# Optimization experiments

Measured on AMD Instinct MI355X. Metric: run time of the kernel, lower is better.

## Reference

```python
import jax, jax.numpy as jnp
import numpy as np

NUM_GAUSS = 64
MAX_R = 5.0
ANG_TO_NM = 0.1  # du.ANG_TO_NM_SCALE
L = 4
C_NODE = 256
C_HID = 256
MAX_ATOMS = 100
B = 512      # building blocks
NPB = 32     # atoms per block
K = 20       # max_neighbors
N = B * NPB
E = N * K
GAUSS_COEFF = -0.5 / (MAX_R / (NUM_GAUSS - 1)) ** 2


def setup_inputs() -> dict:
    rng = np.random.default_rng(0)
    # all atoms of a block inside a 2.5A cube -> every pair within MAX_R=5A,
    # so radius_graph capped at K neighbors == K-nearest graph (fixed E).
    pos = (rng.random((B, NPB, 3)) * 2.5).astype(np.float32)
    d = np.linalg.norm(pos[:, :, None, :] - pos[:, None, :, :], axis=-1)  # [B,n,n]
    ii = np.arange(NPB)
    d[:, ii, ii] = np.inf  # loop=False
    nbr = np.argsort(d, axis=-1)[:, :, :K]  # [B,n,K] nearest neighbors
    base = (np.arange(B) * NPB)[:, None, None]
    row = np.broadcast_to(ii[None, :, None], (B, NPB, K)) + base
    col = nbr + base
    edge_index = np.stack([row.reshape(-1), col.reshape(-1)]).astype(np.int64)

    key = jax.random.key(0)
    ks = jax.random.split(key, 8)

    def lin(k, fi, fo):
        return jax.random.normal(k, (L, fi, fo), jnp.float32) / np.sqrt(fi).astype(np.float32)

    d_e_in = 2 * C_NODE + 1 + NUM_GAUSS  # 577
    return {
        'local_coords': jnp.asarray(pos.reshape(N, 3)),
        'atom_types': jax.random.randint(ks[0], (N,), 1, MAX_ATOMS + 1),  # 1..max_atoms
        'edge_index': jnp.asarray(edge_index),
        'batch_bb': jnp.repeat(jnp.arange(B, dtype=jnp.int32), NPB),
        'atom_embed': jax.random.normal(ks[1], (MAX_ATOMS, C_NODE), jnp.float32) * 0.1,
        'offset': jnp.linspace(0.0, MAX_R, NUM_GAUSS, dtype=jnp.float32),
        'We1': lin(ks[2], d_e_in, C_HID), 'be1': jnp.zeros((L, C_HID), jnp.float32),
        'We2': lin(ks[3], C_HID, C_HID), 'be2': jnp.zeros((L, C_HID), jnp.float32),
        'Wn1': lin(ks[4], C_HID + C_NODE, C_HID), 'bn1': jnp.zeros((L, C_HID), jnp.float32),
        'Wn2': lin(ks[5], C_HID, C_NODE), 'bn2': jnp.zeros((L, C_NODE), jnp.float32),
    }


def _forward(local_coords, atom_types, edge_index, batch_bb, atom_embed, offset,
             We1, be1, We2, be2, Wn1, bn1, Wn2, bn2):
    row, col = edge_index[0], edge_index[1]
    h = atom_embed[atom_types - 1]                      # [N, C_NODE]
    # Gaussian smearing of pairwise distances (Angstrom)
    dvec = local_coords[col] - local_coords[row]        # [E, 3]
    dist = jnp.sqrt(jnp.sum(dvec * dvec, axis=-1))      # [E]
    edge_attr = jnp.exp(GAUSS_COEFF * (dist[:, None] - offset[None, :]) ** 2)  # [E, 64]
    coord = local_coords * ANG_TO_NM
    cdiff = coord[row] - coord[col]
    radial = jnp.sum(cdiff * cdiff, axis=-1, keepdims=True)  # [E, 1]
    nblocks = batch_bb.shape[0] // NPB  # static
    for l in range(L):  # small fixed layer count
        e_in = jnp.concatenate([h[row], h[col], radial, edge_attr], axis=-1)  # [E, 577]
        m = jax.nn.relu(e_in @ We1[l] + be1[l])
        m = jax.nn.relu(m @ We2[l] + be2[l])                 # edge_mlp output [E, C_HID]
        agg = jax.ops.segment_sum(m, row, num_segments=N)    # scatter-sum to nodes
        n_in = jnp.concatenate([h, agg], axis=-1)            # [N, C_NODE + C_HID]
        out = jax.nn.relu(n_in @ Wn1[l] + bn1[l]) @ Wn2[l] + bn2[l]
        node_update = h + out                                # residual inside E_GCL
        h = h + node_update                                  # outer residual in forward
    # global_mean_pool over building blocks
    s = jax.ops.segment_sum(h, batch_bb, num_segments=B)
    cnt = jax.ops.segment_sum(jnp.ones((h.shape[0], 1), h.dtype), batch_bb, num_segments=B)
    return s / cnt


def reference(local_coords, atom_types, edge_index, batch_bb, atom_embed, offset,
              We1, be1, We2, be2, Wn1, bn1, Wn2, bn2):
    return _forward(local_coords, atom_types, edge_index, batch_bb, atom_embed, offset,
                    We1, be1, We2, be2, Wn1, bn1, Wn2, bn2)
```

## Files before the change

### kernel.cpp

```cpp
#include <hip/hip_runtime.h>
#include <hip/hip_bf16.h>
#include <stdint.h>

#define NATOMS 16384
#define ETOT   327680
#define NLAYER 4

typedef __hip_bfloat16 bf16;
using bf16x8 = __attribute__((ext_vector_type(8))) short;
using bf16x4 = __attribute__((ext_vector_type(4))) short;
using f32x4  = __attribute__((ext_vector_type(4))) float;

#define LDSF_STRIDE 260

__device__ __forceinline__ float bf2f(short s) {
  union { float f; unsigned u; } x; x.u = ((unsigned)(unsigned short)s) << 16; return x.f;
}
__device__ __forceinline__ short f2bf(float f) {
  bf16 b = __float2bfloat16(f);
  return *(short*)&b;
}

__device__ __forceinline__ void async16(const void* g, void* l) {
  __builtin_amdgcn_global_load_lds(
      (const __attribute__((address_space(1))) unsigned int*)g,
      (__attribute__((address_space(3))) unsigned int*)l, 16, 0, 0);
}

template<int KTOT, int EPI, int MT>
__global__ void __launch_bounds__(256, 2)
gemm_k(const bf16* A, const bf16* A2, const bf16* B,
       bf16* Obf, int ldOut, const float* bias,
       float* Hf, bf16* Hbf)
{
  __shared__ __align__(16) char smem[49152];
  __shared__ float s_bias[256];

  const int tid  = threadIdx.x;
  const int w    = tid >> 6;
  const int lane = tid & 63;
  const int q    = lane >> 4;
  const int t16  = lane & 15;
  const size_t row0 = (size_t)blockIdx.x * MT;
  const int ncol0 = blockIdx.y * 256;
  constexpr int MI = MT / 16;
  constexpr int AI = MT / 32;

  if constexpr (EPI == 2 || EPI == 4) s_bias[tid] = bias[tid];

  f32x4 acc[MI][4] = {};

  constexpr int NCHUNK = KTOT / 64;
  for (int kc = 0; kc < NCHUNK; ++kc) {
    const int k0 = kc * 64;
    const bf16* Asrc; int k0e; int ldA;
    if constexpr (KTOT == 512) {
      if (k0 < 256) { Asrc = A;  k0e = k0;       }
      else          { Asrc = A2; k0e = k0 - 256; }
      ldA = 256;
    } else {
      Asrc = A; k0e = k0; ldA = KTOT;
    }

    __syncthreads();
    #pragma unroll
    for (int ii = 0; ii < AI; ++ii) {
      int i = w * AI + ii;
      int f = i * 64 + lane;
      int m = f >> 3, s = f & 7;
      int ko = s ^ (m & 7);
      const bf16* g = Asrc + (row0 + (size_t)m) * ldA + (size_t)(k0e + ko * 8);
      async16(g, smem + i * 1024);
    }
    #pragma unroll
    for (int ii = 0; ii < 8; ++ii) {
      int i = w * 8 + ii;
      int f = i * 64 + lane;
      int n = f >> 3, s = f & 7;
      int ko = s ^ (n & 7);
      const bf16* g = B + (size_t)(ncol0 + n) * KTOT + (size_t)(k0 + ko * 8);
      async16(g, smem + 16384 + i * 1024);
    }
    __syncthreads();

    #pragma unroll
    for (int ks = 0; ks < 2; ++ks) {
      bf16x8 av[MI]; bf16x8 bv[4];
      const int ko = q + 4 * ks;
      #pragma unroll
      for (int mi = 0; mi < MI; ++mi) {
        int m = 16 * mi + t16;
        int f = m * 8 + (ko ^ (m & 7));
        av[mi] = *(const bf16x8*)(smem + f * 16);
      }
      #pragma unroll
      for (int ni = 0; ni < 4; ++ni) {
        int n = 64 * w + 16 * ni + t16;
        int f = n * 8 + (ko ^ (n & 7));
        bv[ni] = *(const bf16x8*)(smem + 16384 + f * 16);
      }
      #pragma unroll
      for (int mi = 0; mi < MI; ++mi)
        #pragma unroll
        for (int ni = 0; ni < 4; ++ni)
          acc[mi][ni] = __builtin_amdgcn_mfma_f32_16x16x32_bf16(
              av[mi], bv[ni], acc[mi][ni], 0, 0, 0);
    }
  }

  float* lds_f = (float*)smem;
  #pragma unroll
  for (int mi = 0; mi < MI; ++mi) {
    __syncthreads();
    #pragma unroll
    for (int ni = 0; ni < 4; ++ni)
      #pragma unroll
      for (int r = 0; r < 4; ++r)
        lds_f[(4 * q + r) * LDSF_STRIDE + 64 * w + 16 * ni + t16] = acc[mi][ni][r];
    __syncthreads();
    #pragma unroll
    for (int j = 0; j < 2; ++j) {
      int task = tid + 256 * j;
      int rr = task >> 5, cg = task & 31;
      int c0 = cg * 8;
      size_t rg = row0 + 16 * mi + rr;
      f32x4 v0 = *(const f32x4*)(lds_f + rr * LDSF_STRIDE + c0);
      f32x4 v1 = *(const f32x4*)(lds_f + rr * LDSF_STRIDE + c0 + 4);
      float v[8] = {v0[0], v0[1], v0[2], v0[3], v1[0], v1[1], v1[2], v1[3]};
      if constexpr (EPI == 0) {
        bf16x8 o;
        #pragma unroll
        for (int k = 0; k < 8; ++k) o[k] = f2bf(v[k]);
        *(bf16x8*)(Obf + rg * ldOut + (ncol0 + c0)) = o;
      } else if constexpr (EPI == 2) {
        bf16x8 o;
        #pragma unroll
        for (int k = 0; k < 8; ++k) o[k] = f2bf(fmaxf(v[k] + s_bias[c0 + k], 0.f));
        *(bf16x8*)(Obf + rg * 256 + c0) = o;
      } else {
        f32x4 h0 = *(const f32x4*)(Hf + rg * 256 + c0);
        f32x4 h1 = *(const f32x4*)(Hf + rg * 256 + c0 + 4);
        float hh[8] = {h0[0], h0[1], h0[2], h0[3], h1[0], h1[1], h1[2], h1[3]};
        bf16x8 o; f32x4 n0, n1;
        #pragma unroll
        for (int k = 0; k < 8; ++k) {
          float hn = 2.f * hh[k] + v[k] + s_bias[c0 + k];
          o[k] = f2bf(hn);
          if (k < 4) n0[k] = hn; else n1[k - 4] = hn;
        }
        *(f32x4*)(Hf + rg * 256 + c0)     = n0;
        *(f32x4*)(Hf + rg * 256 + c0 + 4) = n1;
        *(bf16x8*)(Hbf + rg * 256 + c0) = o;
      }
    }
  }
}

#define WINC 40960
#define WINR 57856
#define SCOL 59968
#define SRAD 60288
#define WPITCH 528

__global__ void __launch_bounds__(256, 2)
edge_fused(const bf16* Wgp_l, const bf16* W2p_l, const float* off,
           const float* pos, const int* eidx, const bf16* Prc,
           const float* be1, const float* wrad, const float* be2, bf16* Agg)
{
  __shared__ __align__(16) char smem[60608];
  int*   s_col = (int*)  (smem + SCOL);
  float* s_rad = (float*)(smem + SRAD);

  const int tid  = threadIdx.x;
  const int w    = tid >> 6;
  const int lane = tid & 63;
  const int q    = lane >> 4;
  const int t16  = lane & 15;
  const int blk  = blockIdx.x;
  const int node0  = (blk >> 3) * 32;
  const int rnode0 = blk * 4;
  const int ebase  = blk * 80;

  bf16x8 wgf[4][2];
  #pragma unroll
  for (int fi = 0; fi < 4; ++fi)
    #pragma unroll
    for (int ks = 0; ks < 2; ++ks)
      wgf[fi][ks] = *(const bf16x8*)(Wgp_l + (size_t)(((fi * 2 + ks) * 4 + w) * 512)
                                     + lane * 8);

  {
    int row = tid >> 3, seg = tid & 7;
    const bf16* src = Prc + (size_t)(node0 + row) * 512 + 256 + seg * 32;
    char* dst = smem + WINC + row * WPITCH + seg * 64;
    #pragma unroll
    for (int j = 0; j < 4; ++j)
      *(bf16x8*)(dst + j * 16) = *(const bf16x8*)(src + j * 8);
  }
  if (tid < 128) {
    int row = tid >> 5, seg = tid & 31;
    *(bf16x8*)(smem + WINR + row * WPITCH + seg * 16) =
        *(const bf16x8*)(Prc + (size_t)(rnode0 + row) * 512 + seg * 8);
  }

  if (tid < 80) {
    int e = ebase + tid;
    int rg = rnode0 + tid / 20;
    int cg = eidx[ETOT + e];
    float dx = pos[cg * 3 + 0] - pos[rg * 3 + 0];
    float dy = pos[cg * 3 + 1] - pos[rg * 3 + 1];
    float dz = pos[cg * 3 + 2] - pos[rg * 3 + 2];
    float d2 = dx * dx + dy * dy + dz * dz;
    s_col[tid] = cg & 31;
    s_rad[tid] = 0.01f * d2;
    float d = sqrtf(d2);
    const float GC = -0.5f / ((5.0f / 63.0f) * (5.0f / 63.0f));
    #pragma unroll
    for (int oct = 0; oct < 8; ++oct) {
      bf16x8 v;
      #pragma unroll
      for (int j = 0; j < 8; ++j) {
        float t = d - off[oct * 8 + j];
        v[j] = f2bf(__expf(GC * t * t));
      }
      int f = tid * 8 + (oct ^ (tid & 7));
      *(bf16x8*)(smem + f * 16) = v;
    }
  }
  __syncthreads();

  f32x4 acc1[4][5] = {};
  #pragma unroll
  for (int ks = 0; ks < 2; ++ks) {
    const int ko = q + 4 * ks;
    bf16x8 gv[5];
    #pragma unroll
    for (int ci = 0; ci < 5; ++ci) {
      int e = 16 * ci + t16;
      int f = e * 8 + (ko ^ (e & 7));
      gv[ci] = *(const bf16x8*)(smem + f * 16);
    }
    #pragma unroll
    for (int fi = 0; fi < 4; ++fi)
      #pragma unroll
      for (int ci = 0; ci < 5; ++ci)
        acc1[fi][ci] = __builtin_amdgcn_mfma_f32_16x16x32_bf16(
            wgf[fi][ks], gv[ci], acc1[fi][ci], 0, 0, 0);
  }
  __syncthreads();

  {
    f32x4 tb[4], tw[4];
    #pragma unroll
    for (int fi = 0; fi < 4; ++fi) {
      int fb = 64 * w + 16 * fi + 4 * q;
      tb[fi] = *(const f32x4*)(be1 + fb);
      tw[fi] = *(const f32x4*)(wrad + fb);
    }
    #pragma unroll
    for (int ci = 0; ci < 5; ++ci) {
      int e = 16 * ci + t16;
      int rl = e / 20;
      int cl = s_col[e];
      float rad = s_rad[e];
      #pragma unroll
      for (int fi = 0; fi < 4; ++fi) {
        int fb = 64 * w + 16 * fi + 4 * q;
        bf16x4 pr = *(const bf16x4*)(smem + WINR + rl * WPITCH + fb * 2);
        bf16x4 pc = *(const bf16x4*)(smem + WINC + cl * WPITCH + fb * 2);
        bf16x4 o;
        #pragma unroll
        for (int r = 0; r < 4; ++r) {
          float val = acc1[fi][ci][r] + tb[fi][r] + rad * tw[fi][r]
                    + bf2f(pr[r]) + bf2f(pc[r]);
          o[r] = f2bf(fmaxf(val, 0.f));
        }
        int u = (16 * w + 4 * fi + q) ^ (e & 14);
        *(bf16x4*)(smem + e * 512 + u * 8) = o;
      }
    }
  }
  __syncthreads();

  f32x4 acc2[5][4] = {};
  #pragma unroll
  for (int kc = 0; kc < 4; ++kc) {
    bf16x8 bv[4][2];
    #pragma unroll
    for (int ni = 0; ni < 4; ++ni)
      #pragma unroll
      for (int ks = 0; ks < 2; ++ks) {
        int frag = kc * 8 + ks * 4 + ni;
        bv[ni][ks] = *(const bf16x8*)(W2p_l + (size_t)((frag * 4 + w) * 512)
                                      + lane * 8);
      }
    #pragma unroll
    for (int ks = 0; ks < 2; ++ks) {
      const int ko = q + 4 * ks;
      bf16x8 av[5];
      #pragma unroll
      for (int mi = 0; mi < 5; ++mi) {
        int e = 16 * mi + t16;
        int ub = (2 * (8 * kc + ko)) ^ (t16 & 14);
        av[mi] = *(const bf16x8*)(smem + e * 512 + ub * 8);
      }
      #pragma unroll
      for (int mi = 0; mi < 5; ++mi)
        #pragma unroll
        for (int ni = 0; ni < 4; ++ni)
          acc2[mi][ni] = __builtin_amdgcn_mfma_f32_16x16x32_bf16(
              av[mi], bv[ni][ks], acc2[mi][ni], 0, 0, 0);
    }
  }

  #pragma unroll
  for (int ni = 0; ni < 4; ++ni) {
    float b = be2[64 * w + 16 * ni + t16];
    float pp[5];
    #pragma unroll
    for (int mi = 0; mi < 5; ++mi) {
      float s = 0.f;
      #pragma unroll
      for (int r = 0; r < 4; ++r) s += fmaxf(acc2[mi][ni][r] + b, 0.f);
      pp[mi] = s;
    }
    #pragma unroll
    for (int nn = 0; nn < 4; ++nn) {
      float s = 0.f;
      #pragma unroll
      for (int mi = 0; mi < 5; ++mi) {
        int g = 4 * mi + q;
        if (g >= 5 * nn && g <= 5 * nn + 4) s += pp[mi];
      }
      s += __shfl_xor(s, 16, 64);
      s += __shfl_xor(s, 32, 64);
      if (q == nn)
        Agg[(size_t)(rnode0 + nn) * 256 + 64 * w + 16 * ni + t16] =
            __float2bfloat16(s);
    }
  }
}

__global__ void wrct_kernel(const float* We1, bf16* WrcT) {
  int idx = blockIdx.x * 256 + threadIdx.x;
  int k = idx & 255, np = (idx >> 8) & 511, l = idx >> 17;
  float v = (np < 256)
      ? We1[((size_t)l * 577 + k) * 256 + np]
      : We1[((size_t)l * 577 + 256 + k) * 256 + (np - 256)];
  WrcT[idx] = __float2bfloat16(v);
}
__global__ void wgp_kernel(const float* We1, bf16* Wgp) {
  int idx = blockIdx.x * 256 + threadIdx.x;
  int i = idx & 16383, l = idx >> 14;
  int j = i & 7, lane = (i >> 3) & 63, w = (i >> 9) & 3, fr = i >> 11;
  int fi = fr >> 1, ks = fr & 1;
  int t16 = lane & 15, q = lane >> 4;
  int g = (q + 4 * ks) * 8 + j;
  int feat = 64 * w + 16 * fi + t16;
  Wgp[idx] = __float2bfloat16(We1[((size_t)l * 577 + 513 + g) * 256 + feat]);
}
__global__ void w2p_kernel(const float* We2, bf16* W2p) {
  int idx = blockIdx.x * 256 + threadIdx.x;
  int i = idx & 65535, l = idx >> 16;
  int j = i & 7, lane = (i >> 3) & 63, w = (i >> 9) & 3, fr = i >> 11;
  int ni = fr & 3, ks = (fr >> 2) & 1, kc = fr >> 3;
  int t16 = lane & 15, q = lane >> 4;
  int k = kc * 64 + (q + 4 * ks) * 8 + j;
  int n = 64 * w + 16 * ni + t16;
  W2p[idx] = __float2bfloat16(We2[((size_t)l * 256 + k) * 256 + n]);
}
__global__ void wrad_kernel(const float* We1, float* wrad) {
  int idx = blockIdx.x * 256 + threadIdx.x;
  int n = idx & 255, l = idx >> 8;
  wrad[idx] = We1[((size_t)l * 577 + 512) * 256 + n];
}
__global__ void trans_kernel(const float* src, bf16* dst, int R, int C) {
  int idx = blockIdx.x * 256 + threadIdx.x;
  int k = idx % R, rest = idx / R;
  int n = rest % C, l = rest / C;
  dst[idx] = __float2bfloat16(src[((size_t)l * R + k) * C + n]);
}

__global__ void h0_kernel(const int* types, const float* emb, float* h, bf16* hbf) {
  int i = blockIdx.x, c = threadIdx.x;
  float v = emb[(size_t)(types[i] - 1) * 256 + c];
  h[(size_t)i * 256 + c] = v;
  hbf[(size_t)i * 256 + c] = __float2bfloat16(v);
}

__global__ void pool_kernel(const float* h, float* out) {
  int b = blockIdx.x, c = threadIdx.x;
  float s = 0.f;
  #pragma unroll
  for (int j = 0; j < 32; ++j) s += h[((size_t)b * 32 + j) * 256 + c];
  out[(size_t)b * 256 + c] = s * (1.0f / 32.0f);
}

extern "C" void kernel_launch(void* const* d_in, const int* in_sizes, int n_in,
                              void* d_out, int out_size, void* d_ws, size_t ws_size,
                              hipStream_t stream) {
  const float* pos   = (const float*)d_in[0];
  const int*   atype = (const int*)  d_in[1];
  const int*   eidx  = (const int*)  d_in[2];
  const float* emb   = (const float*)d_in[4];
  const float* off   = (const float*)d_in[5];
  const float* We1   = (const float*)d_in[6];
  const float* be1   = (const float*)d_in[7];
  const float* We2   = (const float*)d_in[8];
  const float* be2   = (const float*)d_in[9];
  const float* Wn1   = (const float*)d_in[10];
  const float* bn1   = (const float*)d_in[11];
  const float* Wn2   = (const float*)d_in[12];
  const float* bn2   = (const float*)d_in[13];
  float* out = (float*)d_out;

  size_t o = 0;
  auto carve = [&](size_t bytes) {
    void* p = (char*)d_ws + o;
    o += (bytes + 255) & ~(size_t)255;
    return p;
  };
  float* h     = (float*)carve((size_t)NATOMS * 256 * 4);
  bf16*  hbf   = (bf16*) carve((size_t)NATOMS * 256 * 2);
  bf16*  Prc   = (bf16*) carve((size_t)NATOMS * 512 * 2);
  bf16*  aggbf = (bf16*) carve((size_t)NATOMS * 256 * 2);
  bf16*  WrcT  = (bf16*) carve((size_t)NLAYER * 512 * 256 * 2);
  bf16*  Wgp   = (bf16*) carve((size_t)NLAYER * 16384 * 2);
  bf16*  W2p   = (bf16*) carve((size_t)NLAYER * 65536 * 2);
  bf16*  Wn1T  = (bf16*) carve((size_t)NLAYER * 256 * 512 * 2);
  bf16*  Wn2T  = (bf16*) carve((size_t)NLAYER * 256 * 256 * 2);
  float* wradp = (float*)carve((size_t)NLAYER * 256 * 4);

  wrct_kernel<<<2048, 256, 0, stream>>>(We1, WrcT);
  wgp_kernel <<< 256, 256, 0, stream>>>(We1, Wgp);
  w2p_kernel <<<1024, 256, 0, stream>>>(We2, W2p);
  wrad_kernel<<<   4, 256, 0, stream>>>(We1, wradp);
  trans_kernel<<<2048, 256, 0, stream>>>(Wn1, Wn1T, 512, 256);
  trans_kernel<<<1024, 256, 0, stream>>>(Wn2, Wn2T, 256, 256);
  h0_kernel  <<<NATOMS, 256, 0, stream>>>(atype, emb, h, hbf);

  for (int l = 0; l < NLAYER; ++l) {
    gemm_k<256, 0, 64><<<dim3(256, 2), 256, 0, stream>>>(
        hbf, nullptr, WrcT + (size_t)l * 512 * 256, Prc, 512, nullptr,
        nullptr, nullptr);
    edge_fused<<<ETOT / 80, 256, 0, stream>>>(
        Wgp + (size_t)l * 16384, W2p + (size_t)l * 65536, off, pos,
        eidx, Prc, be1 + l * 256, wradp + l * 256, be2 + l * 256, aggbf);
    gemm_k<512, 2, 64><<<dim3(256, 1), 256, 0, stream>>>(
        hbf, aggbf, Wn1T + (size_t)l * 256 * 512, aggbf, 256, bn1 + l * 256,
        nullptr, nullptr);
    gemm_k<256, 4, 64><<<dim3(256, 1), 256, 0, stream>>>(
        aggbf, nullptr, Wn2T + (size_t)l * 256 * 256, nullptr, 0, bn2 + l * 256,
        h, hbf);
  }

  pool_kernel<<<512, 256, 0, stream>>>(h, out);
}
```

Baseline: 602.2 us.

## Fuse node MLP and next-layer projection into one kernel, fold edge bias

Replaces the two per-layer node GEMM launches and the next layer's row/col projection GEMM with a single node_fused kernel. It keeps the hidden activation and the updated node features in LDS, and writes Prc for the next layer directly. The edge bias be1 is folded into the projection output so the edge kernel no longer adds it. This removes launches and global round-trips of intermediates, at the cost of a larger LDS footprint and less occupancy per block.

```diff
diff --git a/kernel.cpp b/kernel.cpp
--- a/kernel.cpp
+++ b/kernel.cpp
@@ -34,8 +34,6 @@
        float* Hf, bf16* Hbf)
 {
   __shared__ __align__(16) char smem[49152];
-  __shared__ float s_bias[256];
-
   const int tid  = threadIdx.x;
   const int w    = tid >> 6;
   const int lane = tid & 63;
@@ -46,22 +44,10 @@
   constexpr int MI = MT / 16;
   constexpr int AI = MT / 32;
 
-  if constexpr (EPI == 2 || EPI == 4) s_bias[tid] = bias[tid];
-
   f32x4 acc[MI][4] = {};
-
   constexpr int NCHUNK = KTOT / 64;
   for (int kc = 0; kc < NCHUNK; ++kc) {
     const int k0 = kc * 64;
-    const bf16* Asrc; int k0e; int ldA;
-    if constexpr (KTOT == 512) {
-      if (k0 < 256) { Asrc = A;  k0e = k0;       }
-      else          { Asrc = A2; k0e = k0 - 256; }
-      ldA = 256;
-    } else {
-      Asrc = A; k0e = k0; ldA = KTOT;
-    }
-
     __syncthreads();
     #pragma unroll
     for (int ii = 0; ii < AI; ++ii) {
@@ -69,8 +55,7 @@
       int f = i * 64 + lane;
       int m = f >> 3, s = f & 7;
       int ko = s ^ (m & 7);
-      const bf16* g = Asrc + (row0 + (size_t)m) * ldA + (size_t)(k0e + ko * 8);
-      async16(g, smem + i * 1024);
+      async16(A + (row0 + (size_t)m) * KTOT + (size_t)(k0 + ko * 8), smem + i * 1024);
     }
     #pragma unroll
     for (int ii = 0; ii < 8; ++ii) {
@@ -78,11 +63,10 @@
       int f = i * 64 + lane;
       int n = f >> 3, s = f & 7;
       int ko = s ^ (n & 7);
-      const bf16* g = B + (size_t)(ncol0 + n) * KTOT + (size_t)(k0 + ko * 8);
-      async16(g, smem + 16384 + i * 1024);
-    }
-    __syncthreads();
-
+      async16(B + (size_t)(ncol0 + n) * KTOT + (size_t)(k0 + ko * 8),
+              smem + 16384 + i * 1024);
+    }
+    __syncthreads();
     #pragma unroll
     for (int ks = 0; ks < 2; ++ks) {
       bf16x8 av[MI]; bf16x8 bv[4];
@@ -127,31 +111,14 @@
       f32x4 v0 = *(const f32x4*)(lds_f + rr * LDSF_STRIDE + c0);
       f32x4 v1 = *(const f32x4*)(lds_f + rr * LDSF_STRIDE + c0 + 4);
       float v[8] = {v0[0], v0[1], v0[2], v0[3], v1[0], v1[1], v1[2], v1[3]};
-      if constexpr (EPI == 0) {
-        bf16x8 o;
-        #pragma unroll
-        for (int k = 0; k < 8; ++k) o[k] = f2bf(v[k]);
-        *(bf16x8*)(Obf + rg * ldOut + (ncol0 + c0)) = o;
-      } else if constexpr (EPI == 2) {
-        bf16x8 o;
-        #pragma unroll
-        for (int k = 0; k < 8; ++k) o[k] = f2bf(fmaxf(v[k] + s_bias[c0 + k], 0.f));
-        *(bf16x8*)(Obf + rg * 256 + c0) = o;
-      } else {
-        f32x4 h0 = *(const f32x4*)(Hf + rg * 256 + c0);
-        f32x4 h1 = *(const f32x4*)(Hf + rg * 256 + c0 + 4);
-        float hh[8] = {h0[0], h0[1], h0[2], h0[3], h1[0], h1[1], h1[2], h1[3]};
-        bf16x8 o; f32x4 n0, n1;
-        #pragma unroll
-        for (int k = 0; k < 8; ++k) {
-          float hn = 2.f * hh[k] + v[k] + s_bias[c0 + k];
-          o[k] = f2bf(hn);
-          if (k < 4) n0[k] = hn; else n1[k - 4] = hn;
-        }
-        *(f32x4*)(Hf + rg * 256 + c0)     = n0;
-        *(f32x4*)(Hf + rg * 256 + c0 + 4) = n1;
-        *(bf16x8*)(Hbf + rg * 256 + c0) = o;
-      }
+      bf16x8 o;
+      #pragma unroll
+      for (int k = 0; k < 8; ++k) {
+        float vv = v[k];
+        if (bias != nullptr && ncol0 == 0) vv += bias[c0 + k];
+        o[k] = f2bf(vv);
+      }
+      *(bf16x8*)(Obf + rg * ldOut + (ncol0 + c0)) = o;
     }
   }
 }
@@ -165,7 +132,7 @@
 __global__ void __launch_bounds__(256, 2)
 edge_fused(const bf16* Wgp_l, const bf16* W2p_l, const float* off,
            const float* pos, const int* eidx, const bf16* Prc,
-           const float* be1, const float* wrad, const float* be2, bf16* Agg)
+           const float* wrad, const float* be2, bf16* Agg)
 {
   __shared__ __align__(16) char smem[60608];
   int*   s_col = (int*)  (smem + SCOL);
@@ -250,13 +217,10 @@
   __syncthreads();
 
   {
-    f32x4 tb[4], tw[4];
-    #pragma unroll
-    for (int fi = 0; fi < 4; ++fi) {
-      int fb = 64 * w + 16 * fi + 4 * q;
-      tb[fi] = *(const f32x4*)(be1 + fb);
-      tw[fi] = *(const f32x4*)(wrad + fb);
-    }
+    f32x4 tw[4];
+    #pragma unroll
+    for (int fi = 0; fi < 4; ++fi)
+      tw[fi] = *(const f32x4*)(wrad + 64 * w + 16 * fi + 4 * q);
     #pragma unroll
     for (int ci = 0; ci < 5; ++ci) {
       int e = 16 * ci + t16;
@@ -271,7 +235,7 @@
         bf16x4 o;
         #pragma unroll
         for (int r = 0; r < 4; ++r) {
-          float val = acc1[fi][ci][r] + tb[fi][r] + rad * tw[fi][r]
+          float val = acc1[fi][ci][r] + rad * tw[fi][r]
                     + bf2f(pr[r]) + bf2f(pc[r]);
           o[r] = f2bf(fmaxf(val, 0.f));
         }
@@ -341,12 +305,245 @@
   }
 }
 
+template<bool DO_PRC>
+__global__ void __launch_bounds__(256)
+node_fused(const bf16* Hbf_in, const bf16* Agg, const bf16* Wn1T_l,
+           const bf16* Wn2p_l, const bf16* Wrcp_n,
+           const float* bn1, const float* bn2, const float* be1_n,
+           float* Hf, bf16* Hbf, bf16* Prc)
+{
+  __shared__ __align__(16) char smem[73728];
+  __shared__ float s_bn1[256];
+  __shared__ float s_bn2[256];
+  char* T = smem + 40960;
+
+  const int tid  = threadIdx.x;
+  const int w    = tid >> 6;
+  const int lane = tid & 63;
+  const int q    = lane >> 4;
+  const int t16  = lane & 15;
+  const size_t row0 = (size_t)blockIdx.x * 64;
+
+  s_bn1[tid] = bn1[tid];
+  s_bn2[tid] = bn2[tid];
+
+  f32x4 acc[4][4] = {};
+  for (int kc = 0; kc < 8; ++kc) {
+    const bf16* Asrc = (kc < 4) ? Hbf_in : Agg;
+    const int k0e = (kc & 3) * 64;
+    __syncthreads();
+    #pragma unroll
+    for (int ii = 0; ii < 2; ++ii) {
+      int i = w * 2 + ii;
+      int f = i * 64 + lane;
+      int m = f >> 3, s = f & 7;
+      int ko = s ^ (m & 7);
+      async16(Asrc + (row0 + (size_t)m) * 256 + (size_t)(k0e + ko * 8),
+              smem + i * 1024);
+    }
+    #pragma unroll
+    for (int ii = 0; ii < 8; ++ii) {
+      int i = w * 8 + ii;
+      int f = i * 64 + lane;
+      int n = f >> 3, s = f & 7;
+      int ko = s ^ (n & 7);
+      async16(Wn1T_l + (size_t)n * 512 + (size_t)(kc * 64 + ko * 8),
+              smem + 8192 + i * 1024);
+    }
+    __syncthreads();
+    #pragma unroll
+    for (int ks = 0; ks < 2; ++ks) {
+      bf16x8 av[4]; bf16x8 bv[4];
+      const int ko = q + 4 * ks;
+      #pragma unroll
+      for (int mi = 0; mi < 4; ++mi) {
+        int m = 16 * mi + t16;
+        int f = m * 8 + (ko ^ (m & 7));
+        av[mi] = *(const bf16x8*)(smem + f * 16);
+      }
+      #pragma unroll
+      for (int ni = 0; ni < 4; ++ni) {
+        int n = 64 * w + 16 * ni + t16;
+        int f = n * 8 + (ko ^ (n & 7));
+        bv[ni] = *(const bf16x8*)(smem + 8192 + f * 16);
+      }
+      #pragma unroll
+      for (int mi = 0; mi < 4; ++mi)
+        #pragma unroll
+        for (int ni = 0; ni < 4; ++ni)
+          acc[mi][ni] = __builtin_amdgcn_mfma_f32_16x16x32_bf16(
+              av[mi], bv[ni], acc[mi][ni], 0, 0, 0);
+    }
+  }
+
+  float* lds_f = (float*)smem;
+  #pragma unroll
+  for (int mi = 0; mi < 4; ++mi) {
+    __syncthreads();
+    #pragma unroll
+    for (int ni = 0; ni < 4; ++ni)
+      #pragma unroll
+      for (int r = 0; r < 4; ++r)
+        lds_f[(4 * q + r) * LDSF_STRIDE + 64 * w + 16 * ni + t16] = acc[mi][ni][r];
+    __syncthreads();
+    #pragma unroll
+    for (int j = 0; j < 2; ++j) {
+      int task = tid + 256 * j;
+      int rr = task >> 5, cg = task & 31;
+      int c0 = cg * 8;
+      int rl = 16 * mi + rr;
+      f32x4 v0 = *(const f32x4*)(lds_f + rr * LDSF_STRIDE + c0);
+      f32x4 v1 = *(const f32x4*)(lds_f + rr * LDSF_STRIDE + c0 + 4);
+      float v[8] = {v0[0], v0[1], v0[2], v0[3], v1[0], v1[1], v1[2], v1[3]};
+      bf16x8 o;
+      #pragma unroll
+      for (int k = 0; k < 8; ++k) o[k] = f2bf(fmaxf(v[k] + s_bn1[c0 + k], 0.f));
+      int s = (cg & 24) | ((cg & 7) ^ (rl & 7));
+      *(bf16x8*)(T + rl * 512 + s * 16) = o;
+    }
+  }
+  __syncthreads();
+
+  f32x4 acc2[4][4] = {};
+  #pragma unroll
+  for (int kc = 0; kc < 4; ++kc) {
+    bf16x8 bv[4][2];
+    #pragma unroll
+    for (int ni = 0; ni < 4; ++ni)
+      #pragma unroll
+      for (int ks = 0; ks < 2; ++ks) {
+        int frag = kc * 8 + ks * 4 + ni;
+        bv[ni][ks] = *(const bf16x8*)(Wn2p_l + (size_t)((frag * 4 + w) * 512)
+                                      + lane * 8);
+      }
+    #pragma unroll
+    for (int ks = 0; ks < 2; ++ks) {
+      const int ko = q + 4 * ks;
+      bf16x8 av[4];
+      #pragma unroll
+      for (int mi = 0; mi < 4; ++mi) {
+        int row = 16 * mi + t16;
+        int s = 8 * kc + (ko ^ (t16 & 7));
+        av[mi] = *(const bf16x8*)(T + row * 512 + s * 16);
+      }
+      #pragma unroll
+      for (int mi = 0; mi < 4; ++mi)
+        #pragma unroll
+        for (int ni = 0; ni < 4; ++ni)
+          acc2[mi][ni] = __builtin_amdgcn_mfma_f32_16x16x32_bf16(
+              av[mi], bv[ni][ks], acc2[mi][ni], 0, 0, 0);
+    }
+  }
+
+  #pragma unroll
+  for (int mi = 0; mi < 4; ++mi) {
+    __syncthreads();
+    #pragma unroll
+    for (int ni = 0; ni < 4; ++ni)
+      #pragma unroll
+      for (int r = 0; r < 4; ++r)
+        lds_f[(4 * q + r) * LDSF_STRIDE + 64 * w + 16 * ni + t16] = acc2[mi][ni][r];
+    __syncthreads();
+    #pragma unroll
+    for (int j = 0; j < 2; ++j) {
+      int task = tid + 256 * j;
+      int rr = task >> 5, cg = task & 31;
+      int c0 = cg * 8;
+      int rl = 16 * mi + rr;
+      size_t rg = row0 + rl;
+      f32x4 v0 = *(const f32x4*)(lds_f + rr * LDSF_STRIDE + c0);
+      f32x4 v1 = *(const f32x4*)(lds_f + rr * LDSF_STRIDE + c0 + 4);
+      float v[8] = {v0[0], v0[1], v0[2], v0[3], v1[0], v1[1], v1[2], v1[3]};
+      f32x4 h0 = *(const f32x4*)(Hf + rg * 256 + c0);
+      f32x4 h1 = *(const f32x4*)(Hf + rg * 256 + c0 + 4);
+      float hh[8] = {h0[0], h0[1], h0[2], h0[3], h1[0], h1[1], h1[2], h1[3]};
+      bf16x8 o; f32x4 n0, n1;
+      #pragma unroll
+      for (int k = 0; k < 8; ++k) {
+        float hn = 2.f * hh[k] + v[k] + s_bn2[c0 + k];
+        o[k] = f2bf(hn);
+        if (k < 4) n0[k] = hn; else n1[k - 4] = hn;
+      }
+      *(f32x4*)(Hf + rg * 256 + c0)     = n0;
+      *(f32x4*)(Hf + rg * 256 + c0 + 4) = n1;
+      *(bf16x8*)(Hbf + rg * 256 + c0) = o;
+      int s = (cg & 24) | ((cg & 7) ^ (rl & 7));
+      *(bf16x8*)(T + rl * 512 + s * 16) = o;
+    }
+  }
+
+  if constexpr (DO_PRC) {
+    __syncthreads();
+    #pragma unroll
+    for (int nh = 0; nh < 2; ++nh) {
+      f32x4 acc3[4][4] = {};
+      #pragma unroll
+      for (int kc = 0; kc < 4; ++kc) {
+        bf16x8 bv[4][2];
+        #pragma unroll
+        for (int ni = 0; ni < 4; ++ni)
+          #pragma unroll
+          for (int ks = 0; ks < 2; ++ks) {
+            int frag = kc * 8 + ks * 4 + ni;
+            bv[ni][ks] = *(const bf16x8*)(Wrcp_n + (size_t)nh * 65536 +
+                                          (size_t)((frag * 4 + w) * 512) + lane * 8);
+          }
+        #pragma unroll
+        for (int ks = 0; ks < 2; ++ks) {
+          const int ko = q + 4 * ks;
+          bf16x8 av[4];
+          #pragma unroll
+          for (int mi = 0; mi < 4; ++mi) {
+            int row = 16 * mi + t16;
+            int s = 8 * kc + (ko ^ (t16 & 7));
+            av[mi] = *(const bf16x8*)(T + row * 512 + s * 16);
+          }
+          #pragma unroll
+          for (int mi = 0; mi < 4; ++mi)
+            #pragma unroll
+            for (int ni = 0; ni < 4; ++ni)
+              acc3[mi][ni] = __builtin_amdgcn_mfma_f32_16x16x32_bf16(
+                  av[mi], bv[ni][ks], acc3[mi][ni], 0, 0, 0);
+        }
+      }
+      #pragma unroll
+      for (int mi = 0; mi < 4; ++mi) {
+        __syncthreads();
+        #pragma unroll
+        for (int ni = 0; ni < 4; ++ni)
+          #pragma unroll
+          for (int r = 0; r < 4; ++r)
+            lds_f[(4 * q + r) * LDSF_STRIDE + 64 * w + 16 * ni + t16] = acc3[mi][ni][r];
+        __syncthreads();
+        #pragma unroll
+        for (int j = 0; j < 2; ++j) {
+          int task = tid + 256 * j;
+          int rr = task >> 5, cg = task & 31;
+          int c0 = cg * 8;
+          size_t rg = row0 + 16 * mi + rr;
+          f32x4 v0 = *(const f32x4*)(lds_f + rr * LDSF_STRIDE + c0);
+          f32x4 v1 = *(const f32x4*)(lds_f + rr * LDSF_STRIDE + c0 + 4);
+          float v[8] = {v0[0], v0[1], v0[2], v0[3], v1[0], v1[1], v1[2], v1[3]};
+          bf16x8 o;
+          #pragma unroll
+          for (int k = 0; k < 8; ++k) {
+            float vv = v[k];
+            if (nh == 0) vv += be1_n[c0 + k];
+            o[k] = f2bf(vv);
+          }
+          *(bf16x8*)(Prc + rg * 512 + nh * 256 + c0) = o;
+        }
+      }
+    }
+  }
+}
+
 __global__ void wrct_kernel(const float* We1, bf16* WrcT) {
   int idx = blockIdx.x * 256 + threadIdx.x;
-  int k = idx & 255, np = (idx >> 8) & 511, l = idx >> 17;
+  int k = idx & 255, np = (idx >> 8) & 511;
   float v = (np < 256)
-      ? We1[((size_t)l * 577 + k) * 256 + np]
-      : We1[((size_t)l * 577 + 256 + k) * 256 + (np - 256)];
+      ? We1[((size_t)k) * 256 + np]
+      : We1[((size_t)256 + k) * 256 + (np - 256)];
   WrcT[idx] = __float2bfloat16(v);
 }
 __global__ void wgp_kernel(const float* We1, bf16* Wgp) {
@@ -359,7 +556,7 @@
   int feat = 64 * w + 16 * fi + t16;
   Wgp[idx] = __float2bfloat16(We1[((size_t)l * 577 + 513 + g) * 256 + feat]);
 }
-__global__ void w2p_kernel(const float* We2, bf16* W2p) {
+__global__ void w2p_kernel(const float* W, bf16* Wp) {
   int idx = blockIdx.x * 256 + threadIdx.x;
   int i = idx & 65535, l = idx >> 16;
   int j = i & 7, lane = (i >> 3) & 63, w = (i >> 9) & 3, fr = i >> 11;
@@ -367,7 +564,17 @@
   int t16 = lane & 15, q = lane >> 4;
   int k = kc * 64 + (q + 4 * ks) * 8 + j;
   int n = 64 * w + 16 * ni + t16;
-  W2p[idx] = __float2bfloat16(We2[((size_t)l * 256 + k) * 256 + n]);
+  Wp[idx] = __float2bfloat16(W[((size_t)l * 256 + k) * 256 + n]);
+}
+__global__ void wrcp_kernel(const float* We1, bf16* Wrcp) {
+  int idx = blockIdx.x * 256 + threadIdx.x;
+  int i = idx & 65535, nh = (idx >> 16) & 1, l = idx >> 17;
+  int j = i & 7, lane = (i >> 3) & 63, w = (i >> 9) & 3, fr = i >> 11;
+  int ni = fr & 3, ks = (fr >> 2) & 1, kc = fr >> 3;
+  int t16 = lane & 15, q = lane >> 4;
+  int k = kc * 64 + (q + 4 * ks) * 8 + j;
+  int n = 64 * w + 16 * ni + t16;
+  Wrcp[idx] = __float2bfloat16(We1[((size_t)l * 577 + nh * 256 + k) * 256 + n]);
 }
 __global__ void wrad_kernel(const float* We1, float* wrad) {
   int idx = blockIdx.x * 256 + threadIdx.x;
@@ -424,34 +631,40 @@
   bf16*  hbf   = (bf16*) carve((size_t)NATOMS * 256 * 2);
   bf16*  Prc   = (bf16*) carve((size_t)NATOMS * 512 * 2);
   bf16*  aggbf = (bf16*) carve((size_t)NATOMS * 256 * 2);
-  bf16*  WrcT  = (bf16*) carve((size_t)NLAYER * 512 * 256 * 2);
+  bf16*  WrcT  = (bf16*) carve((size_t)512 * 256 * 2);
   bf16*  Wgp   = (bf16*) carve((size_t)NLAYER * 16384 * 2);
   bf16*  W2p   = (bf16*) carve((size_t)NLAYER * 65536 * 2);
   bf16*  Wn1T  = (bf16*) carve((size_t)NLAYER * 256 * 512 * 2);
-  bf16*  Wn2T  = (bf16*) carve((size_t)NLAYER * 256 * 256 * 2);
+  bf16*  Wn2p  = (bf16*) carve((size_t)NLAYER * 65536 * 2);
+  bf16*  Wrcp  = (bf16*) carve((size_t)NLAYER * 2 * 65536 * 2);
   float* wradp = (float*)carve((size_t)NLAYER * 256 * 4);
 
-  wrct_kernel<<<2048, 256, 0, stream>>>(We1, WrcT);
+  wrct_kernel<<< 512, 256, 0, stream>>>(We1, WrcT);
   wgp_kernel <<< 256, 256, 0, stream>>>(We1, Wgp);
   w2p_kernel <<<1024, 256, 0, stream>>>(We2, W2p);
+  w2p_kernel <<<1024, 256, 0, stream>>>(Wn2, Wn2p);
+  wrcp_kernel<<<2048, 256, 0, stream>>>(We1, Wrcp);
   wrad_kernel<<<   4, 256, 0, stream>>>(We1, wradp);
   trans_kernel<<<2048, 256, 0, stream>>>(Wn1, Wn1T, 512, 256);
-  trans_kernel<<<1024, 256, 0, stream>>>(Wn2, Wn2T, 256, 256);
   h0_kernel  <<<NATOMS, 256, 0, stream>>>(atype, emb, h, hbf);
 
+  gemm_k<256, 0, 64><<<dim3(256, 2), 256, 0, stream>>>(
+      hbf, nullptr, WrcT, Prc, 512, be1, nullptr, nullptr);
+
   for (int l = 0; l < NLAYER; ++l) {
-    gemm_k<256, 0, 64><<<dim3(256, 2), 256, 0, stream>>>(
-        hbf, nullptr, WrcT + (size_t)l * 512 * 256, Prc, 512, nullptr,
-        nullptr, nullptr);
     edge_fused<<<ETOT / 80, 256, 0, stream>>>(
         Wgp + (size_t)l * 16384, W2p + (size_t)l * 65536, off, pos,
-        eidx, Prc, be1 + l * 256, wradp + l * 256, be2 + l * 256, aggbf);
-    gemm_k<512, 2, 64><<<dim3(256, 1), 256, 0, stream>>>(
-        hbf, aggbf, Wn1T + (size_t)l * 256 * 512, aggbf, 256, bn1 + l * 256,
-        nullptr, nullptr);
-    gemm_k<256, 4, 64><<<dim3(256, 1), 256, 0, stream>>>(
-        aggbf, nullptr, Wn2T + (size_t)l * 256 * 256, nullptr, 0, bn2 + l * 256,
-        h, hbf);
+        eidx, Prc, wradp + l * 256, be2 + l * 256, aggbf);
+    if (l < NLAYER - 1) {
+      node_fused<true><<<256, 256, 0, stream>>>(
+          hbf, aggbf, Wn1T + (size_t)l * 131072, Wn2p + (size_t)l * 65536,
+          Wrcp + (size_t)(l + 1) * 131072, bn1 + l * 256, bn2 + l * 256,
+          be1 + (l + 1) * 256, h, hbf, Prc);
+    } else {
+      node_fused<false><<<256, 256, 0, stream>>>(
+          hbf, aggbf, Wn1T + (size_t)l * 131072, Wn2p + (size_t)l * 65536,
+          nullptr, bn1 + l * 256, bn2 + l * 256, nullptr, h, hbf, nullptr);
+    }
   }
 
   pool_kernel<<<512, 256, 0, stream>>>(h, out);
```

Result: no change. 607.0 us (+0.8%).
